# Kernel tuning notes

Hardware: AMD Instinct MI355X
Metric: run time of the kernel (lower is better)

## Reference

```python
import jax, jax.numpy as jnp
import numpy as np

N = 8192
IN_FEATS = 512
OUT_FEATS = 512


def setup_inputs() -> dict:
    key = jax.random.key(0)
    k_adj, k_feat, k_w = jax.random.split(key, 3)
    adj = jax.random.uniform(k_adj, (N, N), dtype=jnp.float32)
    features = jax.random.normal(k_feat, (N, IN_FEATS), dtype=jnp.float32)
    # nn.Linear(in_feats, out_feats, bias=False): weight is [out, in]; we store transposed [in, out]
    W = jax.random.normal(k_w, (IN_FEATS, OUT_FEATS), dtype=jnp.float32) / np.sqrt(IN_FEATS)
    return {"adj": adj, "features": features, "W": W}


def reference(adj, features, W):
    n = adj.shape[0]
    # adj + I (self loops)
    a = adj + jnp.eye(n, dtype=adj.dtype)
    # symmetric degree normalization D^{-1/2} A D^{-1/2}
    deg = jnp.sum(a, axis=1)  # [N]
    d_inv_sqrt = jnp.where(deg > 0, jax.lax.rsqrt(deg), 0.0)  # inf -> 0 as in torch code
    # diag(d) @ a @ diag(d) == d[:,None] * a * d[None,:] (algebraic simplification of O(N^3) diag matmuls)
    norm_adj = d_inv_sqrt[:, None] * a * d_inv_sqrt[None, :]  # [N, N]
    h = norm_adj @ features  # [N, in]
    return h @ W  # [N, out]
```

## Files before the change

kernel.cpp:

```cpp
#include <hip/hip_runtime.h>
#include <cstdint>
#include <cstddef>

#define NN 8192
#define NF 512
#define SPLITK 4

typedef __attribute__((ext_vector_type(8))) short bf16x8;
typedef __attribute__((ext_vector_type(8))) unsigned short u16x8;
typedef __attribute__((ext_vector_type(4))) float f32x4;

__device__ __forceinline__ unsigned short f2bf_bits(float f) {
  unsigned u = __builtin_bit_cast(unsigned, f);
  u += 0x7FFFu + ((u >> 16) & 1u);
  return (unsigned short)(u >> 16);
}

__device__ __forceinline__ float bf2f(unsigned short b) {
  return __builtin_bit_cast(float, (unsigned)b << 16);
}

__device__ __forceinline__ bf16x8 cvt8(float4 a, float4 b) {
  bf16x8 r;
  r[0] = (short)f2bf_bits(a.x); r[1] = (short)f2bf_bits(a.y);
  r[2] = (short)f2bf_bits(a.z); r[3] = (short)f2bf_bits(a.w);
  r[4] = (short)f2bf_bits(b.x); r[5] = (short)f2bf_bits(b.y);
  r[6] = (short)f2bf_bits(b.z); r[7] = (short)f2bf_bits(b.w);
  return r;
}

__device__ __forceinline__ void gld_lds16(const void* g, void* l) {
  __builtin_amdgcn_global_load_lds(
      (const __attribute__((address_space(1))) unsigned int*)g,
      (__attribute__((address_space(3))) unsigned int*)l, 16, 0, 0);
}

template <bool CVT>
__global__ void k_rowsum(const float* __restrict__ adj, float* __restrict__ dinv,
                         short* __restrict__ adjb) {
  const int row = blockIdx.x;
  const float4* p = (const float4*)(adj + (size_t)row * NN);
  short* ob = CVT ? (adjb + (size_t)row * NN) : nullptr;
  float s = 0.f;
#pragma unroll
  for (int j = 0; j < 8; ++j) {
    float4 v = p[j * 256 + threadIdx.x];
    s += (v.x + v.y) + (v.z + v.w);
    if (CVT) {
      ushort4 o;
      o.x = f2bf_bits(v.x); o.y = f2bf_bits(v.y);
      o.z = f2bf_bits(v.z); o.w = f2bf_bits(v.w);
      *(ushort4*)&ob[(size_t)(j * 256 + threadIdx.x) * 4] = o;
    }
  }
#pragma unroll
  for (int off = 32; off > 0; off >>= 1) s += __shfl_down(s, off, 64);
  __shared__ float red[4];
  if ((threadIdx.x & 63) == 0) red[threadIdx.x >> 6] = s;
  __syncthreads();
  if (threadIdx.x == 0) {
    float deg = red[0] + red[1] + red[2] + red[3] + 1.0f;
    dinv[row] = (deg > 0.f) ? (1.0f / sqrtf(deg)) : 0.f;
  }
}

__global__ void k_transpose2(const float* __restrict__ feat, const float* __restrict__ W,
                             const float* __restrict__ dinv,
                             short* __restrict__ FbT, short* __restrict__ WbT) {
  __shared__ float tile[32][33];
  const bool isF = (blockIdx.y < (NN / 32));
  const float* src = isF ? feat : W;
  short* dst = isF ? FbT : WbT;
  const int rows = isF ? NN : NF;
  const int r0 = (isF ? blockIdx.y : (blockIdx.y - NN / 32)) * 32;
  const int c0 = blockIdx.x * 32;
  const int tx = threadIdx.x & 31, ty = threadIdx.x >> 5;
#pragma unroll
  for (int i = 0; i < 32; i += 8) {
    float v = src[(size_t)(r0 + ty + i) * NF + c0 + tx];
    if (isF) v *= dinv[r0 + ty + i];
    tile[ty + i][tx] = v;
  }
  __syncthreads();
#pragma unroll
  for (int i = 0; i < 32; i += 8)
    dst[(size_t)(c0 + ty + i) * rows + r0 + tx] = (short)f2bf_bits(tile[tx][ty + i]);
}

__global__ __launch_bounds__(512, 1)
void k_gemm8(const short* __restrict__ Ab, const short* __restrict__ Bt,
             int N, int K, unsigned short* __restrict__ Pout) {
  __shared__ __align__(16) short As[3][2][256 * 32];
  __shared__ __align__(16) short Bs[2][2][256 * 32];
  const int tid = threadIdx.x, lane = tid & 63, w = tid >> 6;
  const int wm = w >> 2, wn = w & 3;

  const int hid = (blockIdx.z * gridDim.y + blockIdx.y) * gridDim.x + blockIdx.x;
  const int xcd = hid & 7, rr = hid >> 3;
  const int pair = xcd * 16 + (rr >> 1);
  const int member = rr & 1;
  const int m0 = (pair & 31) * 256;
  const int n0 = member * 256;
  const int kz = pair >> 5;
  const int ksl = K / SPLITK;
  const int kbase = kz * ksl;
  const int nt = ksl >> 6;
  unsigned short* Cp = Pout + (size_t)kz * ((size_t)NN * (size_t)N);

  f32x4 acc[8][4];
#pragma unroll
  for (int m = 0; m < 8; ++m)
#pragma unroll
    for (int n = 0; n < 4; ++n) acc[m][n] = (f32x4){0.f, 0.f, 0.f, 0.f};

  const int lr = lane & 15, kg = lane >> 4;

  auto stageA = [&](int buf, int t) {
#pragma unroll
    for (int h = 0; h < 2; ++h) {
      const int kofs = kbase + (t << 6) + (h << 5) + ((lane & 3) << 3);
#pragma unroll
      for (int rnd = 0; rnd < 2; ++rnd) {
        const int rowb = (rnd << 7) + (w << 4);
        const int row = rowb + (lane >> 2);
        gld_lds16(Ab + (size_t)(m0 + row) * K + kofs, &As[buf][h][rowb << 5]);
      }
    }
  };
  auto stageB = [&](int buf, int t) {
#pragma unroll
    for (int h = 0; h < 2; ++h) {
      const int kofs = kbase + (t << 6) + (h << 5) + ((lane & 3) << 3);
#pragma unroll
      for (int rnd = 0; rnd < 2; ++rnd) {
        const int rowb = (rnd << 7) + (w << 4);
        const int row = rowb + (lane >> 2);
        gld_lds16(Bt + (size_t)(n0 + row) * K + kofs, &Bs[buf][h][rowb << 5]);
      }
    }
  };
  auto readA = [&](int buf, int kh, bf16x8* a) {
#pragma unroll
    for (int mf = 0; mf < 8; ++mf)
      a[mf] = *(const bf16x8*)&As[buf][kh][(((wm << 7) + (mf << 4) + lr) << 5) + (kg << 3)];
  };
  auto readB2 = [&](int buf, int kh, int nh, bf16x8* b) {
#pragma unroll
    for (int i = 0; i < 2; ++i)
      b[i] = *(const bf16x8*)&Bs[buf][kh][(((wn << 6) + (((nh << 1) + i) << 4) + lr) << 5) + (kg << 3)];
  };
  auto mfma16 = [&](bf16x8* a, bf16x8* b, int nh) {
#pragma unroll
    for (int mf = 0; mf < 8; ++mf)
#pragma unroll
      for (int i = 0; i < 2; ++i)
        acc[mf][(nh << 1) + i] =
            __builtin_amdgcn_mfma_f32_16x16x32_bf16(a[mf], b[i], acc[mf][(nh << 1) + i], 0, 0, 0);
  };

  stageA(0, 0);
  stageB(0, 0);
  stageA(1, 1);

  for (int t = 0; t < nt; ++t) {
    const int ab = t % 3, bb = t & 1;
    bf16x8 a[8], b0[2], b1[2];
    if (t + 1 < nt) asm volatile("s_waitcnt vmcnt(4)" ::: "memory");
    else            asm volatile("s_waitcnt vmcnt(0)" ::: "memory");
    __builtin_amdgcn_s_barrier();
    __builtin_amdgcn_sched_barrier(0);
    readA(ab, 0, a);
    readB2(bb, 0, 0, b0);
    if (t + 1 < nt) stageB((t + 1) & 1, t + 1);
    asm volatile("s_waitcnt lgkmcnt(0)" ::: "memory");
    __builtin_amdgcn_sched_barrier(0);
    __builtin_amdgcn_s_setprio(1);
    mfma16(a, b0, 0);
    __builtin_amdgcn_s_setprio(0);
    __builtin_amdgcn_sched_barrier(0);
    readB2(bb, 0, 1, b1);
    asm volatile("s_waitcnt lgkmcnt(0)" ::: "memory");
    __builtin_amdgcn_sched_barrier(0);
    __builtin_amdgcn_s_setprio(1);
    mfma16(a, b1, 1);
    __builtin_amdgcn_s_setprio(0);
    __builtin_amdgcn_sched_barrier(0);
    readA(ab, 1, a);
    readB2(bb, 1, 0, b0);
    if (t + 2 < nt) stageA((t + 2) % 3, t + 2);
    asm volatile("s_waitcnt lgkmcnt(0)" ::: "memory");
    __builtin_amdgcn_sched_barrier(0);
    __builtin_amdgcn_s_setprio(1);
    mfma16(a, b0, 0);
    __builtin_amdgcn_s_setprio(0);
    __builtin_amdgcn_sched_barrier(0);
    readB2(bb, 1, 1, b1);
    asm volatile("s_waitcnt lgkmcnt(0)" ::: "memory");
    __builtin_amdgcn_sched_barrier(0);
    __builtin_amdgcn_s_setprio(1);
    mfma16(a, b1, 1);
    __builtin_amdgcn_s_setprio(0);
    __builtin_amdgcn_sched_barrier(0);
  }

  const int cl = lane & 15, rg = lane >> 4;
#pragma unroll
  for (int mf = 0; mf < 8; ++mf)
#pragma unroll
    for (int nf = 0; nf < 4; ++nf)
#pragma unroll
      for (int j = 0; j < 4; ++j) {
        const int gi = m0 + (wm << 7) + (mf << 4) + (rg << 2) + j;
        const int gn = n0 + (wn << 6) + (nf << 4) + cl;
        Cp[(size_t)gi * N + gn] = f2bf_bits(acc[mf][nf][j]);
      }
}

template <int MODE>
__global__ __launch_bounds__(512, 2)
void k_gemm2(const void* __restrict__ Ap, const short* __restrict__ Bt,
             int N, int K,
             const float* __restrict__ dinv, const float* __restrict__ feat,
             void* __restrict__ Cp) {
  __shared__ __align__(16) short As[4][128 * 64];
  __shared__ __align__(16) short Bs[4][128 * 64];
  const int tid = threadIdx.x;
  const int lane = tid & 63;
  const int w = tid >> 6;
  const int wm = (w >> 1) & 1, wn = w & 1, kk = w >> 2;

  const int bid = blockIdx.y * gridDim.x + blockIdx.x;
  const int nb = gridDim.x * gridDim.y;
  const int sbid = ((nb & 7) == 0) ? ((bid & 7) * (nb >> 3) + (bid >> 3)) : bid;
  const int n0 = (sbid % gridDim.x) * 128;
  const int m0 = (sbid / gridDim.x) * 128;
  const int nt = K >> 6;

  f32x4 acc[4][4];
#pragma unroll
  for (int m = 0; m < 4; ++m)
#pragma unroll
    for (int n = 0; n < 4; ++n) acc[m][n] = (f32x4){0.f, 0.f, 0.f, 0.f};

  const int lr = lane & 15, kg = lane >> 4;
  const int lc = (kk << 2) + kg;

  auto stage_b = [&](int buf, int t) {
    const int kofs = t << 6;
#pragma unroll
    for (int q = 0; q < 2; ++q) {
      const int rblk = (w << 4) + (q << 3);
      const int r = rblk + (lane >> 3);
      const int sc = (lane & 7) ^ (r & 7);
      gld_lds16(Bt + (size_t)(n0 + r) * K + kofs + (sc << 3), &Bs[buf][rblk << 6]);
    }
  };
  auto stage_a = [&](int buf, int t) {
    const int kofs = t << 6;
    const short* Ab = (const short*)Ap;
#pragma unroll
    for (int q = 0; q < 2; ++q) {
      const int rblk = (w << 4) + (q << 3);
      const int r = rblk + (lane >> 3);
      const int sc = (lane & 7) ^ (r & 7);
      gld_lds16(Ab + (size_t)(m0 + r) * K + kofs + (sc << 3), &As[buf][rblk << 6]);
    }
  };
  auto stage_a_f32 = [&](int buf, int t) {
    const int kofs = t << 6;
    const float* Af = (const float*)Ap;
    const int r = tid >> 2;
    const int c0 = (tid & 3) << 4;
    const float* s = Af + (size_t)(m0 + r) * K + kofs + c0;
    float4 x0 = ((const float4*)s)[0], x1 = ((const float4*)s)[1];
    float4 x2 = ((const float4*)s)[2], x3 = ((const float4*)s)[3];
    const int cc = (tid & 3) << 1;
    *(bf16x8*)&As[buf][(r << 6) + ((cc ^ (r & 7)) << 3)]       = cvt8(x0, x1);
    *(bf16x8*)&As[buf][(r << 6) + (((cc + 1) ^ (r & 7)) << 3)] = cvt8(x2, x3);
  };
  auto stage_a_fused = [&](int buf, int t) {
    const int kofs = t << 6;
    const unsigned short* Pp = (const unsigned short*)Ap;
    const int r = tid >> 2;
    const int c0 = (tid & 3) << 4;
    const int gi = m0 + r;
    const size_t base = (size_t)gi * K + kofs + c0;
    const size_t str = (size_t)NN * NF;
    float s[16];
#pragma unroll
    for (int j = 0; j < 16; ++j) s[j] = 0.f;
#pragma unroll
    for (int kz = 0; kz < SPLITK; ++kz) {
      u16x8 v0 = *(const u16x8*)&Pp[kz * str + base];
      u16x8 v1 = *(const u16x8*)&Pp[kz * str + base + 8];
#pragma unroll
      for (int j = 0; j < 8; ++j) { s[j] += bf2f(v0[j]); s[8 + j] += bf2f(v1[j]); }
    }
    const float d = dinv[gi], d2 = d * d;
    float h[16];
#pragma unroll
    for (int j = 0; j < 16; ++j) h[j] = d * s[j] + d2 * feat[base + j];
    float4 h0 = {h[0], h[1], h[2], h[3]},   h1 = {h[4], h[5], h[6], h[7]};
    float4 h2 = {h[8], h[9], h[10], h[11]}, h3 = {h[12], h[13], h[14], h[15]};
    const int cc = (tid & 3) << 1;
    *(bf16x8*)&As[buf][(r << 6) + ((cc ^ (r & 7)) << 3)]       = cvt8(h0, h1);
    *(bf16x8*)&As[buf][(r << 6) + (((cc + 1) ^ (r & 7)) << 3)] = cvt8(h2, h3);
  };
  auto read_a = [&](int buf, bf16x8* a) {
#pragma unroll
    for (int m = 0; m < 4; ++m) {
      const int r = (wm << 6) + (m << 4) + lr;
      a[m] = *(const bf16x8*)&As[buf][(r << 6) + ((lc ^ (r & 7)) << 3)];
    }
  };
  auto read_b2 = [&](int buf, int nh, bf16x8* b) {
#pragma unroll
    for (int i = 0; i < 2; ++i) {
      const int r = (wn << 6) + (((nh << 1) + i) << 4) + lr;
      b[i] = *(const bf16x8*)&Bs[buf][(r << 6) + ((lc ^ (r & 7)) << 3)];
    }
  };
  auto mfma8 = [&](bf16x8* a, bf16x8* b, int nh) {
#pragma unroll
    for (int m = 0; m < 4; ++m)
#pragma unroll
      for (int i = 0; i < 2; ++i)
        acc[m][(nh << 1) + i] =
            __builtin_amdgcn_mfma_f32_16x16x32_bf16(a[m], b[i], acc[m][(nh << 1) + i], 0, 0, 0);
  };

  if constexpr (MODE == 0) {
    stage_a(0, 0); stage_b(0, 0);
    stage_a(1, 1); stage_b(1, 1);
    asm volatile("s_waitcnt vmcnt(4)" ::: "memory");
    __builtin_amdgcn_s_barrier();
    __builtin_amdgcn_sched_barrier(0);
    for (int t = 0; t < nt; ++t) {
      const int cur = t & 3;
      const bool more = (t + 2 < nt);
      bf16x8 a[4], b0[2], b1[2];
      read_a(cur, a);
      read_b2(cur, 0, b0);
      if (more) stage_a((t + 2) & 3, t + 2);
      __builtin_amdgcn_s_barrier();
      asm volatile("s_waitcnt lgkmcnt(0)" ::: "memory");
      __builtin_amdgcn_sched_barrier(0);
      __builtin_amdgcn_s_setprio(1);
      mfma8(a, b0, 0);
      __builtin_amdgcn_s_setprio(0);
      __builtin_amdgcn_sched_barrier(0);
      read_b2(cur, 1, b1);
      if (more) stage_b((t + 2) & 3, t + 2);
      asm volatile("s_waitcnt lgkmcnt(0)" ::: "memory");
      __builtin_amdgcn_sched_barrier(0);
      __builtin_amdgcn_s_setprio(1);
      mfma8(a, b1, 1);
      __builtin_amdgcn_s_setprio(0);
      __builtin_amdgcn_sched_barrier(0);
      if (more)            asm volatile("s_waitcnt vmcnt(4)" ::: "memory");
      else if (t + 1 < nt) asm volatile("s_waitcnt vmcnt(0)" ::: "memory");
      __builtin_amdgcn_s_barrier();
      __builtin_amdgcn_sched_barrier(0);
    }
  } else {
    if constexpr (MODE == 1) { stage_a_f32(0, 0); stage_a_f32(1, 1); }
    else                     { stage_a_fused(0, 0); stage_a_fused(1, 1); }
    stage_b(0, 0); stage_b(1, 1);
    __syncthreads();
    for (int t = 0; t < nt; ++t) {
      const int cur = t & 3;
      if (t + 2 < nt) {
        if constexpr (MODE == 1) stage_a_f32((t + 2) & 3, t + 2);
        else                     stage_a_fused((t + 2) & 3, t + 2);
        stage_b((t + 2) & 3, t + 2);
      }
      bf16x8 a[4], b0[2], b1[2];
      read_a(cur, a); read_b2(cur, 0, b0); read_b2(cur, 1, b1);
      __builtin_amdgcn_s_setprio(1);
      mfma8(a, b0, 0); mfma8(a, b1, 1);
      __builtin_amdgcn_s_setprio(0);
      __syncthreads();
    }
  }

  __syncthreads();
  float* red = (float*)&As[0][0];
  if (w >= 4) {
    float* my = red + ((w - 4) << 12);
#pragma unroll
    for (int m = 0; m < 4; ++m)
#pragma unroll
      for (int n = 0; n < 4; ++n)
        *(f32x4*)&my[(((m << 2) + n) << 8) + (lane << 2)] = acc[m][n];
  }
  __syncthreads();
  if (w < 4) {
    float* my = red + (w << 12);
#pragma unroll
    for (int m = 0; m < 4; ++m)
#pragma unroll
      for (int n = 0; n < 4; ++n)
        acc[m][n] += *(const f32x4*)&my[(((m << 2) + n) << 8) + (lane << 2)];
    const int cl = lane & 15, rg = lane >> 4;
#pragma unroll
    for (int m = 0; m < 4; ++m)
#pragma unroll
      for (int n = 0; n < 4; ++n)
#pragma unroll
        for (int j = 0; j < 4; ++j) {
          const int gi = m0 + (wm << 6) + (m << 4) + (rg << 2) + j;
          const int gn = n0 + (wn << 6) + (n << 4) + cl;
          const float v = acc[m][n][j];
          if constexpr (MODE == 1) {
            const float d = dinv[gi];
            const float hv = d * v + d * d * feat[(size_t)gi * NF + gn];
            ((unsigned short*)Cp)[(size_t)gi * N + gn] = f2bf_bits(hv);
          } else {
            ((float*)Cp)[(size_t)gi * N + gn] = v;
          }
        }
  }
}

extern "C" void kernel_launch(void* const* d_in, const int* in_sizes, int n_in,
                              void* d_out, int out_size, void* d_ws, size_t ws_size,
                              hipStream_t stream) {
  const float* adj  = (const float*)d_in[0];
  const float* feat = (const float*)d_in[1];
  const float* W    = (const float*)d_in[2];

  char* ws = (char*)d_ws;
  float* dinv = (float*)ws;
  short* FbT  = (short*)(ws + 32768);
  short* WbT  = (short*)(ws + 32768 + 8388608);
  short* Hb   = (short*)(ws + 32768 + 8388608 + 524288);
  short* adjb = (short*)(ws + 32768 + 8388608 + 524288 + 8388608);
  unsigned short* part = (unsigned short*)(ws + 32768 + 8388608 + 524288 + 8388608 + 134217728);
  float* out  = (float*)d_out;
  const size_t need = (size_t)32768 + 8388608 + 524288 + 8388608 + 134217728 +
                      (size_t)SPLITK * NN * NF * 2;
  const bool big_ws = ws_size >= need;

  if (big_ws) {
    k_rowsum<true><<<NN, 256, 0, stream>>>(adj, dinv, adjb);
  } else {
    k_rowsum<false><<<NN, 256, 0, stream>>>(adj, dinv, nullptr);
  }
  k_transpose2<<<dim3(NF / 32, NN / 32 + NF / 32), 256, 0, stream>>>(feat, W, dinv, FbT, WbT);

  if (big_ws) {
    k_gemm8<<<dim3(NF / 256, NN / 256, SPLITK), 512, 0, stream>>>(adjb, FbT, NF, NN, part);
    k_gemm2<2><<<dim3(NF / 128, NN / 128), 512, 0, stream>>>(
        part, WbT, NF, NF, dinv, feat, out);
  } else {
    k_gemm2<1><<<dim3(NF / 128, NN / 128), 512, 0, stream>>>(
        adj, FbT, NF, NN, dinv, feat, Hb);
    k_gemm2<0><<<dim3(NF / 128, NN / 128), 512, 0, stream>>>(
        Hb, WbT, NF, NF, nullptr, nullptr, out);
  }
}
```

Measured before the change: 172.3 us.

## Load fp32 adjacency directly in split-K GEMM, converting to bf16 in registers

The row-sum kernel no longer writes a bf16 copy of the adjacency matrix. Instead the main split-K GEMM reads fp32 adj straight from global memory into registers, converts it to bf16, and writes it into LDS with an XOR swizzle. This removes a 128MB write and a 128MB re-read of the bf16 copy. In exchange the GEMM reads twice the bytes for A, the A loads go through registers rather than direct global-to-LDS loads, and the pipeline now waits on vmcnt(0) every iteration, which weakens load/compute overlap.

```diff
diff --git a/kernel.cpp b/kernel.cpp
--- a/kernel.cpp
+++ b/kernel.cpp
@@ -88,7 +88,7 @@
 }
 
 __global__ __launch_bounds__(512, 1)
-void k_gemm8(const short* __restrict__ Ab, const short* __restrict__ Bt,
+void k_gemm8(const float* __restrict__ Af, const short* __restrict__ Bt,
              int N, int K, unsigned short* __restrict__ Pout) {
   __shared__ __align__(16) short As[3][2][256 * 32];
   __shared__ __align__(16) short Bs[2][2][256 * 32];
@@ -115,17 +115,20 @@
 
   const int lr = lane & 15, kg = lane >> 4;
 
-  auto stageA = [&](int buf, int t) {
-#pragma unroll
-    for (int h = 0; h < 2; ++h) {
-      const int kofs = kbase + (t << 6) + (h << 5) + ((lane & 3) << 3);
-#pragma unroll
-      for (int rnd = 0; rnd < 2; ++rnd) {
-        const int rowb = (rnd << 7) + (w << 4);
-        const int row = rowb + (lane >> 2);
-        gld_lds16(Ab + (size_t)(m0 + row) * K + kofs, &As[buf][h][rowb << 5]);
-      }
-    }
+  const int arow = tid >> 1, ahalf = tid & 1;
+  const float* aptr = Af + (size_t)(m0 + arow) * K + kbase + ahalf * 32;
+
+  float4 av[8];
+  auto issueA = [&](int t) {
+    const float* s = aptr + (t << 6);
+#pragma unroll
+    for (int j = 0; j < 8; ++j) av[j] = ((const float4*)s)[j];
+  };
+  auto writeA = [&](int buf) {
+    short* dst = &As[buf][ahalf][arow << 5];
+#pragma unroll
+    for (int j = 0; j < 4; ++j)
+      *(bf16x8*)&dst[(j ^ (arow & 3)) << 3] = cvt8(av[2 * j], av[2 * j + 1]);
   };
   auto stageB = [&](int buf, int t) {
 #pragma unroll
@@ -141,8 +144,10 @@
   };
   auto readA = [&](int buf, int kh, bf16x8* a) {
 #pragma unroll
-    for (int mf = 0; mf < 8; ++mf)
-      a[mf] = *(const bf16x8*)&As[buf][kh][(((wm << 7) + (mf << 4) + lr) << 5) + (kg << 3)];
+    for (int mf = 0; mf < 8; ++mf) {
+      const int row = (wm << 7) + (mf << 4) + lr;
+      a[mf] = *(const bf16x8*)&As[buf][kh][(row << 5) + ((kg ^ (row & 3)) << 3)];
+    }
   };
   auto readB2 = [&](int buf, int kh, int nh, bf16x8* b) {
 #pragma unroll
@@ -158,19 +163,21 @@
             __builtin_amdgcn_mfma_f32_16x16x32_bf16(a[mf], b[i], acc[mf][(nh << 1) + i], 0, 0, 0);
   };
 
-  stageA(0, 0);
+  issueA(0);
   stageB(0, 0);
-  stageA(1, 1);
+  writeA(0);
+  issueA(1);
+  writeA(1);
 
   for (int t = 0; t < nt; ++t) {
     const int ab = t % 3, bb = t & 1;
     bf16x8 a[8], b0[2], b1[2];
-    if (t + 1 < nt) asm volatile("s_waitcnt vmcnt(4)" ::: "memory");
-    else            asm volatile("s_waitcnt vmcnt(0)" ::: "memory");
+    asm volatile("s_waitcnt vmcnt(0) lgkmcnt(0)" ::: "memory");
     __builtin_amdgcn_s_barrier();
     __builtin_amdgcn_sched_barrier(0);
     readA(ab, 0, a);
     readB2(bb, 0, 0, b0);
+    if (t + 2 < nt) issueA(t + 2);
     if (t + 1 < nt) stageB((t + 1) & 1, t + 1);
     asm volatile("s_waitcnt lgkmcnt(0)" ::: "memory");
     __builtin_amdgcn_sched_barrier(0);
@@ -187,7 +194,6 @@
     __builtin_amdgcn_sched_barrier(0);
     readA(ab, 1, a);
     readB2(bb, 1, 0, b0);
-    if (t + 2 < nt) stageA((t + 2) % 3, t + 2);
     asm volatile("s_waitcnt lgkmcnt(0)" ::: "memory");
     __builtin_amdgcn_sched_barrier(0);
     __builtin_amdgcn_s_setprio(1);
@@ -201,6 +207,7 @@
     mfma16(a, b1, 1);
     __builtin_amdgcn_s_setprio(0);
     __builtin_amdgcn_sched_barrier(0);
+    if (t + 2 < nt) writeA((t + 2) % 3);
   }
 
   const int cl = lane & 15, rg = lane >> 4;
@@ -434,22 +441,17 @@
   short* FbT  = (short*)(ws + 32768);
   short* WbT  = (short*)(ws + 32768 + 8388608);
   short* Hb   = (short*)(ws + 32768 + 8388608 + 524288);
-  short* adjb = (short*)(ws + 32768 + 8388608 + 524288 + 8388608);
   unsigned short* part = (unsigned short*)(ws + 32768 + 8388608 + 524288 + 8388608 + 134217728);
   float* out  = (float*)d_out;
   const size_t need = (size_t)32768 + 8388608 + 524288 + 8388608 + 134217728 +
                       (size_t)SPLITK * NN * NF * 2;
   const bool big_ws = ws_size >= need;
 
+  k_rowsum<false><<<NN, 256, 0, stream>>>(adj, dinv, nullptr);
+  k_transpose2<<<dim3(NF / 32, NN / 32 + NF / 32), 256, 0, stream>>>(feat, W, dinv, FbT, WbT);
+
   if (big_ws) {
-    k_rowsum<true><<<NN, 256, 0, stream>>>(adj, dinv, adjb);
-  } else {
-    k_rowsum<false><<<NN, 256, 0, stream>>>(adj, dinv, nullptr);
-  }
-  k_transpose2<<<dim3(NF / 32, NN / 32 + NF / 32), 256, 0, stream>>>(feat, W, dinv, FbT, WbT);
-
-  if (big_ws) {
-    k_gemm8<<<dim3(NF / 256, NN / 256, SPLITK), 512, 0, stream>>>(adjb, FbT, NF, NN, part);
+    k_gemm8<<<dim3(NF / 256, NN / 256, SPLITK), 512, 0, stream>>>(adj, FbT, NF, NN, part);
     k_gemm2<2><<<dim3(NF / 128, NN / 128), 512, 0, stream>>>(
         part, WbT, NF, NF, dinv, feat, out);
   } else {
```

After: 208.4 us. 21.0% more time.
